# Optimization experiments

Hardware: AMD Instinct MI355X
Metric: run time of the kernel (lower is better)

## Reference

```python
import jax, jax.numpy as jnp
import numpy as np

B_SZ, SEQ = 16, 2048
VOCAB, EMBED = 50257, 128
DSTATE, HID, NCLS = 16, 256, 10
NEDGE = 8192  # edges per graph (avg degree 4)
LN_EPS = 1e-5


def setup_inputs() -> dict:
    key = jax.random.key(0)
    ks = jax.random.split(key, 12)
    tokens = jax.random.randint(ks[0], (B_SZ, SEQ), 0, VOCAB, dtype=jnp.int32)
    lengths = jnp.full((B_SZ,), SEQ, dtype=jnp.int32)  # full-length graphs
    edge_indices = jax.random.randint(ks[1], (B_SZ, 2, NEDGE), 0, SEQ, dtype=jnp.int32)
    emb = (jax.random.normal(ks[2], (VOCAB, EMBED)) * 0.02).at[0].set(0.0)  # padding_idx=0
    A_log = jax.random.normal(ks[3], (EMBED, DSTATE)) * 0.1
    B_w = jax.random.normal(ks[4], (DSTATE, EMBED)) * (1.0 / np.sqrt(EMBED))
    C_w = jax.random.normal(ks[5], (EMBED, DSTATE)) * (1.0 / np.sqrt(DSTATE))
    D_skip = jnp.ones((EMBED,))
    ln_g = jnp.ones((EMBED,))
    ln_b = jnp.zeros((EMBED,))
    Wmsg_w = jax.random.normal(ks[6], (HID, EMBED)) * (1.0 / np.sqrt(EMBED))
    Wupd_w = jax.random.normal(ks[7], (HID, EMBED + HID)) * (1.0 / np.sqrt(EMBED + HID))
    Wupd_b = jax.random.normal(ks[8], (HID,)) * 0.01
    cls_w = jax.random.normal(ks[9], (NCLS, HID)) * (1.0 / np.sqrt(HID))
    cls_b = jnp.zeros((NCLS,))
    return {"tokens": tokens, "lengths": lengths, "edge_indices": edge_indices,
            "emb": emb, "A_log": A_log, "B_w": B_w, "C_w": C_w, "D_skip": D_skip,
            "ln_g": ln_g, "ln_b": ln_b, "Wmsg_w": Wmsg_w, "Wupd_w": Wupd_w,
            "Wupd_b": Wupd_b, "cls_w": cls_w, "cls_b": cls_b}


def _ssm(x, A_log, B_w, C_w, D_skip, ln_g, ln_b):
    # x: (B, S, d_model). Diagonal SSM: h_t = h_{t-1}*exp(A) + B x_t (broadcast over d_model)
    Aexp = jnp.exp(-jnp.exp(A_log))  # (d_model, d_state)
    h0 = jnp.zeros((x.shape[0], EMBED, DSTATE), dtype=x.dtype)

    def step(h, x_t):  # x_t: (B, d_model)
        b_t = x_t @ B_w.T                            # (B, d_state)
        h = h * Aexp[None] + b_t[:, None, :]          # (B, d_model, d_state)
        y = h.mean(axis=1) @ C_w.T + D_skip * x_t     # (B, d_model)
        return h, y

    _, ys = jax.lax.scan(step, h0, jnp.swapaxes(x, 0, 1))
    out = jnp.swapaxes(ys, 0, 1)                      # (B, S, d_model)
    mu = out.mean(-1, keepdims=True)
    var = jnp.mean((out - mu) ** 2, axis=-1, keepdims=True)
    return ln_g * (out - mu) * jax.lax.rsqrt(var + LN_EPS) + ln_b


def reference(tokens, lengths, edge_indices, emb, A_log, B_w, C_w, D_skip,
              ln_g, ln_b, Wmsg_w, Wupd_w, Wupd_b, cls_w, cls_b):
    x = emb[tokens]                                   # (B, S, E)
    h = _ssm(x, A_log, B_w, C_w, D_skip, ln_g, ln_b)  # (B, S, E)
    src, dst = edge_indices[:, 0, :], edge_indices[:, 1, :]   # (B, Ne)
    h_src = jnp.take_along_axis(h, src[:, :, None], axis=1)   # (B, Ne, E)
    msgs = jnp.einsum('bed,hd->beh', h_src, Wmsg_w)            # (B, Ne, H)
    flat_dst = (jnp.arange(B_SZ, dtype=dst.dtype)[:, None] * SEQ + dst).reshape(-1)
    agg = jax.ops.segment_sum(msgs.reshape(-1, HID), flat_dst,
                              num_segments=B_SZ * SEQ).reshape(B_SZ, SEQ, HID)
    upd = jax.nn.relu(jnp.concatenate([h, agg], axis=-1) @ Wupd_w.T + Wupd_b)  # (B, S, H)
    pooled = upd.mean(axis=1)                          # (B, H)  (all lengths == SEQ)
    return pooled @ cls_w.T + cls_b                    # (B, NCLS)
```

## Files before the change

kernel.cpp:

```cpp
#include <hip/hip_runtime.h>

#define B_SZ   16
#define SEQ    2048
#define VOCAB  50257
#define EMBED  128
#define DSTATE 16
#define HID    256
#define NCLS   10
#define NEDGE  8192
#define KTR    64
#define LN_EPS 1e-5f
#define NROW   (B_SZ*SEQ)
#define BCAP   32
#define OVCAP  1024

#define PB_PRECM  128
#define PB_CTAB   (PB_PRECM + 16)
#define PB_TOTAL  (PB_CTAB + 1)

typedef float  f32x4 __attribute__((ext_vector_type(4)));
typedef short  s16x8 __attribute__((ext_vector_type(8)));

__device__ __forceinline__ float scrub(float x){
  return (x == x && fabsf(x) < 1e30f) ? x : 0.f;
}
__device__ __forceinline__ short f2b(float f){
  unsigned int u = __float_as_uint(f);
  unsigned int r = (u + 0x7fffu + ((u >> 16) & 1u)) >> 16;
  return (short)r;
}
__device__ __forceinline__ unsigned int pack2(float a, float b){
  return (unsigned int)(unsigned short)f2b(a)
       | ((unsigned int)(unsigned short)f2b(b) << 16);
}
__device__ __forceinline__ float lo2f(unsigned int v){ return __uint_as_float(v << 16); }
__device__ __forceinline__ float hi2f(unsigned int v){ return __uint_as_float(v & 0xffff0000u); }

__global__ __launch_bounds__(256) void k_prep(
    const float* __restrict__ A_log, const float* __restrict__ B_w,
    const float* __restrict__ Wmsg, const float* __restrict__ Wupd,
    float* __restrict__ c_tab, short* __restrict__ Bf, float* __restrict__ MT){
  int bid = blockIdx.x, tid = threadIdx.x;
  if (bid < PB_PRECM){
    int hp = bid*2 + (tid >> 7);
    int e  = tid & 127;
    const float* w2 = Wupd + (size_t)hp*384 + 128;
    float acc = 0.f;
    for (int h1 = 0; h1 < HID; ++h1)
      acc += Wmsg[h1*EMBED + e] * w2[h1];
    MT[(size_t)hp*EMBED + e] = scrub(acc);
  } else if (bid < PB_CTAB){
    if (tid < 64){
      int d = bid - PB_PRECM, lane = tid;
      float a0 = scrub(expf(-expf(A_log[(2*lane+0)*DSTATE + d])));
      float a1 = scrub(expf(-expf(A_log[(2*lane+1)*DSTATE + d])));
      float p0 = 1.f, p1 = 1.f;
      for (int k = 0; k < KTR; ++k){
        float s = p0 + p1;
        for (int off = 32; off; off >>= 1) s += __shfl_down(s, off);
        if (lane == 0) c_tab[k*DSTATE + d] = scrub(s * (1.0f/128.0f));
        p0 *= a0; p1 *= a1;
      }
    }
  } else {
    int idx = tid;
    int c = idx >> 6, lane = idx & 63;
    int n = lane & 15;
    int kb = c*32 + (lane >> 4)*8;
    short v[8];
    #pragma unroll
    for (int jj = 0; jj < 8; ++jj) v[jj] = f2b(B_w[(size_t)n*EMBED + kb + jj]);
    *(s16x8*)(Bf + (size_t)idx*8) = *(s16x8*)v;
  }
}

__global__ __launch_bounds__(256) void k_ssm_fused(
    const int* __restrict__ tokens, const float* __restrict__ emb,
    const float* __restrict__ c_tab,
    const float* __restrict__ C_w, const float* __restrict__ D_skip,
    const float* __restrict__ ln_g, const float* __restrict__ ln_b,
    const short* __restrict__ Bf, const float* __restrict__ Wupd,
    const float* __restrict__ MT, unsigned int* __restrict__ h_out,
    short* __restrict__ Wcs, const int* __restrict__ edges,
    int* __restrict__ cnt, unsigned short* __restrict__ bucket,
    int* __restrict__ ovf_cnt, int* __restrict__ ovf){
  __shared__ unsigned int xsh[128][68];
  __shared__ float bsh[128][18];
  __shared__ float msh[64][18];
  __shared__ float Ct[DSTATE][EMBED+2];
  __shared__ float csh[KTR][DSTATE];
  int bid = blockIdx.x, tid = threadIdx.x;

  if (bid >= 544){
    int eid = (bid-544)*256 + tid;
    int b2 = eid >> 13, i = eid & (NEDGE-1);
    const int* ei = edges + (size_t)b2*2*NEDGE;
    int s = ei[i]         & (SEQ-1);
    int d = ei[NEDGE + i] & (SEQ-1);
    int gdst = (b2 << 11) | d;
    int slot = atomicAdd(&cnt[gdst], 1);
    if (slot < BCAP) bucket[(size_t)gdst*BCAP + slot] = (unsigned short)s;
    else {
      int o = atomicAdd(ovf_cnt, 1);
      if (o < OVCAP) ovf[o] = ((b2 << 11) | s) | (gdst << 16);
    }
    return;
  }

  if (bid >= 512){
    int idx = (bid-512)*256 + tid;
    int c    = idx >> 10;
    int rem  = idx & 1023;
    int j    = rem >> 6;
    int lane = rem & 63;
    int n  = j*16 + (lane & 15);
    int kb = c*32 + (lane >> 4)*8;
    short v[8];
    #pragma unroll
    for (int jj = 0; jj < 8; ++jj){
      int k = kb + jj;
      float val = (k < 128) ? Wupd[(size_t)n*384 + k] : MT[(size_t)n*EMBED + (k-128)];
      v[jj] = f2b(val);
    }
    *(s16x8*)(Wcs + (size_t)idx*8) = *(s16x8*)v;
    return;
  }

  int b  = bid >> 5;
  int t0 = (bid & 31) * 64;

  {
    const int* tkb = tokens + b*SEQ;
    for (int i = 0; i < 16; ++i){
      int gid = i*256 + tid;
      int lr = gid >> 5, ch = gid & 31;
      int t = t0 - 64 + lr;
      uint2 o; o.x = 0u; o.y = 0u;
      if (t >= 0){
        int tok = tkb[t];
        tok = tok < 0 ? 0 : (tok >= VOCAB ? VOCAB-1 : tok);
        float4 v = *(const float4*)(emb + (size_t)tok*EMBED + ch*4);
        o.x = pack2(v.x, v.y); o.y = pack2(v.z, v.w);
      }
      *(uint2*)&xsh[lr][ch*2] = o;
    }
  }
  for (int i = tid; i < DSTATE*EMBED; i += 256){
    int e = i >> 4, d = i & 15;
    Ct[d][e] = C_w[i];
  }
  for (int i = tid; i < KTR*DSTATE; i += 256)
    csh[i >> 4][i & 15] = c_tab[i];
  __syncthreads();

  int wv = tid >> 6, lane = tid & 63;
  int m = lane & 15, lg = lane >> 4;

  const s16x8* Bp = (const s16x8*)Bf;
  #pragma unroll
  for (int tt = 0; tt < 2; ++tt){
    int tile = wv*2 + tt;
    int trow = t0 - 64 + tile*16;
    f32x4 acc = (f32x4){0.f,0.f,0.f,0.f};
    if (trow >= 0){
      const short* xrow = (const short*)&xsh[tile*16 + m][0] + lg*8;
      #pragma unroll
      for (int c = 0; c < 4; ++c){
        s16x8 a = *(const s16x8*)(xrow + c*32);
        acc = __builtin_amdgcn_mfma_f32_16x16x32_bf16(a, Bp[c*64 + lane], acc, 0, 0, 0);
      }
    }
    #pragma unroll
    for (int r = 0; r < 4; ++r)
      bsh[tile*16 + lg*4 + r][m] = scrub(acc[r]);
  }
  __syncthreads();

  {
    int d = tid & 15;
    #pragma unroll
    for (int it = 0; it < 4; ++it){
      int q = (tid + it*256) >> 4;
      int t = t0 + q;
      int base = 64 + q;
      int kmax = (t+1 < KTR) ? t+1 : KTR;
      float acc = 0.f;
      for (int k = 0; k < kmax; ++k) acc += csh[k][d] * bsh[base-k][d];
      msh[q][d] = scrub(acc);
    }
  }
  __syncthreads();

  int e0 = lane*2;
  float2 dsk = *(const float2*)&D_skip[e0];
  float2 lgv = *(const float2*)&ln_g[e0];
  float2 lbv = *(const float2*)&ln_b[e0];
  for (int q = wv*16; q < wv*16+16; ++q){
    int row = b*SEQ + t0 + q;
    unsigned int xp = xsh[64 + q][lane];
    float x0 = lo2f(xp), x1 = hi2f(xp);
    float y0 = dsk.x*x0, y1 = dsk.y*x1;
    #pragma unroll
    for (int d = 0; d < DSTATE; ++d){
      float md = msh[q][d];
      y0 += md * Ct[d][e0];
      y1 += md * Ct[d][e0+1];
    }
    y0 = scrub(y0); y1 = scrub(y1);
    float s = y0+y1, s2 = y0*y0 + y1*y1;
    for (int off = 32; off; off >>= 1){ s += __shfl_down(s,off); s2 += __shfl_down(s2,off); }
    s = __shfl(s, 0); s2 = __shfl(s2, 0);
    float mu  = s * (1.f/EMBED);
    float var = s2 * (1.f/EMBED) - mu*mu;
    float inv = rsqrtf(fmaxf(var, 0.f) + LN_EPS);
    float o0 = scrub(lgv.x*(y0-mu)*inv + lbv.x);
    float o1 = scrub(lgv.y*(y1-mu)*inv + lbv.y);
    h_out[(size_t)row*(EMBED/2) + lane] = pack2(o0, o1);
  }
}

__global__ __launch_bounds__(256) void k_gupd(
    const short* __restrict__ h, const int* __restrict__ cnt,
    const unsigned short* __restrict__ bucket,
    const int* __restrict__ ovf_cnt, const int* __restrict__ ovf,
    const short* __restrict__ Wcs, const float* __restrict__ Wupd_b,
    const float* __restrict__ cls_w, const float* __restrict__ cls_b,
    float* __restrict__ out){
  __shared__ unsigned int gsh[16][68];
  __shared__ float psum[HID];
  __shared__ float oacc[4][NCLS];
  int tid = threadIdx.x;
  int wv = tid >> 6, lane = tid & 63;
  int row0 = blockIdx.x * 16;
  int b = row0 >> 11;
  int m = lane & 15, lg = lane >> 4;

  const unsigned int* hb  = (const unsigned int*)h + (size_t)b*SEQ*(EMBED/2);
  const unsigned int* h32 = (const unsigned int*)h;
  int on = *ovf_cnt; on = on > OVCAP ? OVCAP : on;
  int hh = lane >> 5;
  int lw = lane & 31;
  for (int i = 0; i < 2; ++i){
    int rloc = wv*4 + i*2 + hh;
    int r = row0 + rloc;
    int n = cnt[r]; n = n > BCAP ? BCAP : n;
    const unsigned short* bk = bucket + (size_t)r*BCAP;
    float ax0=0.f, ay0=0.f, ax1=0.f, ay1=0.f;
    int t = 0;
    for (; t + 4 <= n; t += 4){
      ushort4 s4 = *(const ushort4*)(bk + t);
      uint2 v0 = *(const uint2*)&hb[(size_t)s4.x*(EMBED/2) + lw*2];
      uint2 v1 = *(const uint2*)&hb[(size_t)s4.y*(EMBED/2) + lw*2];
      uint2 v2 = *(const uint2*)&hb[(size_t)s4.z*(EMBED/2) + lw*2];
      uint2 v3 = *(const uint2*)&hb[(size_t)s4.w*(EMBED/2) + lw*2];
      ax0 += lo2f(v0.x); ay0 += hi2f(v0.x); ax1 += lo2f(v0.y); ay1 += hi2f(v0.y);
      ax0 += lo2f(v1.x); ay0 += hi2f(v1.x); ax1 += lo2f(v1.y); ay1 += hi2f(v1.y);
      ax0 += lo2f(v2.x); ay0 += hi2f(v2.x); ax1 += lo2f(v2.y); ay1 += hi2f(v2.y);
      ax0 += lo2f(v3.x); ay0 += hi2f(v3.x); ax1 += lo2f(v3.y); ay1 += hi2f(v3.y);
    }
    for (; t < n; ++t){
      uint2 v = *(const uint2*)&hb[(size_t)bk[t]*(EMBED/2) + lw*2];
      ax0 += lo2f(v.x); ay0 += hi2f(v.x); ax1 += lo2f(v.y); ay1 += hi2f(v.y);
    }
    for (int idx = 0; idx < on; ++idx){
      int pk = ovf[idx];
      if (((pk >> 16) & 0x7fff) == r){
        uint2 v = *(const uint2*)&h32[(size_t)(pk & 0xffff)*(EMBED/2) + lw*2];
        ax0 += lo2f(v.x); ay0 += hi2f(v.x); ax1 += lo2f(v.y); ay1 += hi2f(v.y);
      }
    }
    uint2 o; o.x = pack2(scrub(ax0), scrub(ay0));
    o.y = pack2(scrub(ax1), scrub(ay1));
    *(uint2*)&gsh[rloc][lw*2] = o;
  }
  __syncthreads();

  const short* hrow = h + (size_t)(row0+m)*EMBED + lg*8;
  s16x8 hfrag[4], gfrag[4];
  #pragma unroll
  for (int c = 0; c < 4; ++c){
    hfrag[c] = *(const s16x8*)(hrow + c*32);
    gfrag[c] = *(const s16x8*)&gsh[m][c*16 + lg*4];
  }

  int j0 = wv*4;
  f32x4 acc[4];
  #pragma unroll
  for (int jj = 0; jj < 4; ++jj) acc[jj] = (f32x4){0.f,0.f,0.f,0.f};
  const s16x8* Bp = (const s16x8*)Wcs;
  #pragma unroll
  for (int c = 0; c < 8; ++c){
    s16x8 a = (c < 4) ? hfrag[c] : gfrag[c-4];
    #pragma unroll
    for (int jj = 0; jj < 4; ++jj){
      s16x8 bfr = Bp[(c*16 + j0 + jj)*64 + lane];
      acc[jj] = __builtin_amdgcn_mfma_f32_16x16x32_bf16(a, bfr, acc[jj], 0, 0, 0);
    }
  }

  #pragma unroll
  for (int jj = 0; jj < 4; ++jj){
    int n = (j0 + jj)*16 + m;
    float bias = Wupd_b[n];
    float v = 0.f;
    #pragma unroll
    for (int r = 0; r < 4; ++r) v += fmaxf(acc[jj][r] + bias, 0.f);
    v += __shfl_down(v, 32);
    v += __shfl_down(v, 16);
    if (lane < 16) psum[n] = scrub(v);
  }
  __syncthreads();

  {
    float pn = psum[tid];
    #pragma unroll
    for (int c = 0; c < NCLS; ++c){
      float t = pn * cls_w[c*HID + tid];
      for (int off = 32; off; off >>= 1) t += __shfl_down(t, off);
      if (lane == 0) oacc[wv][c] = t;
    }
    __syncthreads();
    if (tid < NCLS){
      float s = oacc[0][tid] + oacc[1][tid] + oacc[2][tid] + oacc[3][tid];
      atomicAdd(&out[b*NCLS + tid], scrub(s * (1.0f/SEQ)));
    }
    if ((blockIdx.x & 127) == 0 && tid < NCLS)
      atomicAdd(&out[b*NCLS + tid], cls_b[tid]);
  }
}

extern "C" void kernel_launch(void* const* d_in, const int* in_sizes, int n_in,
                              void* d_out, int out_size, void* d_ws, size_t ws_size,
                              hipStream_t stream) {
  const int*   tokens = (const int*)d_in[0];
  const int*   edges  = (const int*)d_in[2];
  const float* emb    = (const float*)d_in[3];
  const float* A_log  = (const float*)d_in[4];
  const float* B_w    = (const float*)d_in[5];
  const float* C_w    = (const float*)d_in[6];
  const float* D_skip = (const float*)d_in[7];
  const float* ln_g   = (const float*)d_in[8];
  const float* ln_b   = (const float*)d_in[9];
  const float* Wmsg   = (const float*)d_in[10];
  const float* Wupd   = (const float*)d_in[11];
  const float* Wupd_b = (const float*)d_in[12];
  const float* cls_w  = (const float*)d_in[13];
  const float* cls_b  = (const float*)d_in[14];
  float* out = (float*)d_out;

  char* ws = (char*)d_ws;
  float* c_tab = (float*)ws;  ws += 16*1024;
  float* MT    = (float*)ws;  ws += (size_t)HID*EMBED*4;
  short* Wcs   = (short*)ws;  ws += (size_t)HID*HID*2;
  short* Bf    = (short*)ws;  ws += 16*1024;
  char*  zbase = ws;
  int*   cnt   = (int*)ws;    ws += (size_t)NROW*4;
  int*   ovf_cnt = (int*)ws;  ws += 64;
  int*   ovf   = (int*)ws;    ws += OVCAP*4;
  size_t zlen = (size_t)((char*)ws - zbase);
  unsigned short* bucket = (unsigned short*)ws; ws += (size_t)NROW*BCAP*2;
  short* h_bf  = (short*)ws;  ws += (size_t)NROW*EMBED*2;

  hipMemsetAsync(zbase, 0, zlen, stream);
  hipMemsetAsync(out, 0, (size_t)B_SZ*NCLS*4, stream);
  hipLaunchKernelGGL(k_prep, dim3(PB_TOTAL), dim3(256), 0, stream,
                     A_log, B_w, Wmsg, Wupd, c_tab, Bf, MT);
  hipLaunchKernelGGL(k_ssm_fused, dim3(1056), dim3(256), 0, stream,
                     tokens, emb, c_tab, C_w, D_skip, ln_g, ln_b, Bf, Wupd, MT,
                     (unsigned int*)h_bf, Wcs, edges, cnt, bucket, ovf_cnt, ovf);
  hipLaunchKernelGGL(k_gupd, dim3(NROW/16), dim3(256), 0, stream,
                     h_bf, cnt, bucket, ovf_cnt, ovf, Wcs, Wupd_b,
                     cls_w, cls_b, out);
}
```

Before: 179.9 us.

## Fold memsets into prep kernel, halve SSM tile size, keep C_w in registers

Replaces the two hipMemsetAsync calls with zeroing blocks inside the prep kernel, which removes two extra stream operations. The SSM main blocks now cover 32 timesteps instead of 64, doubling the block count to 1024 for better occupancy, at the cost of a proportionally larger 64-step halo reload per block. The C_w transpose in shared memory is replaced by per-thread register copies loaded straight from global memory. The zeroing covers cnt, ovf_cnt and ovf via a computed int count, so correctness depends on that size matching.

```diff
diff --git a/kernel.cpp b/kernel.cpp
--- a/kernel.cpp
+++ b/kernel.cpp
@@ -16,7 +16,15 @@
 
 #define PB_PRECM  128
 #define PB_CTAB   (PB_PRECM + 16)
-#define PB_TOTAL  (PB_CTAB + 1)
+#define PB_PRECB  (PB_CTAB + 1)
+#define PB_ZNINT  33808
+#define PB_ZBLK   34
+#define PB_ZOUT   (PB_PRECB + PB_ZBLK)
+#define PB_TOTAL  (PB_ZOUT + 1)
+
+#define SSM_MAIN  1024
+#define SSM_PRECW (SSM_MAIN + 32)
+#define SSM_TOTAL (SSM_PRECW + 512)
 
 typedef float  f32x4 __attribute__((ext_vector_type(4)));
 typedef short  s16x8 __attribute__((ext_vector_type(8)));
@@ -39,7 +47,8 @@
 __global__ __launch_bounds__(256) void k_prep(
     const float* __restrict__ A_log, const float* __restrict__ B_w,
     const float* __restrict__ Wmsg, const float* __restrict__ Wupd,
-    float* __restrict__ c_tab, short* __restrict__ Bf, float* __restrict__ MT){
+    float* __restrict__ c_tab, short* __restrict__ Bf, float* __restrict__ MT,
+    int* __restrict__ cnt, float* __restrict__ out){
   int bid = blockIdx.x, tid = threadIdx.x;
   if (bid < PB_PRECM){
     int hp = bid*2 + (tid >> 7);
@@ -62,7 +71,7 @@
         p0 *= a0; p1 *= a1;
       }
     }
-  } else {
+  } else if (bid < PB_PRECB){
     int idx = tid;
     int c = idx >> 6, lane = idx & 63;
     int n = lane & 15;
@@ -71,6 +80,14 @@
     #pragma unroll
     for (int jj = 0; jj < 8; ++jj) v[jj] = f2b(B_w[(size_t)n*EMBED + kb + jj]);
     *(s16x8*)(Bf + (size_t)idx*8) = *(s16x8*)v;
+  } else if (bid < PB_ZOUT){
+    int idx4 = (bid-PB_PRECB)*1024 + tid*4;
+    if (idx4 < PB_ZNINT){
+      uint4 z; z.x = z.y = z.z = z.w = 0u;
+      *(uint4*)&cnt[idx4] = z;
+    }
+  } else {
+    if (tid < B_SZ*NCLS) out[tid] = 0.f;
   }
 }
 
@@ -84,15 +101,14 @@
     short* __restrict__ Wcs, const int* __restrict__ edges,
     int* __restrict__ cnt, unsigned short* __restrict__ bucket,
     int* __restrict__ ovf_cnt, int* __restrict__ ovf){
-  __shared__ unsigned int xsh[128][68];
-  __shared__ float bsh[128][18];
-  __shared__ float msh[64][18];
-  __shared__ float Ct[DSTATE][EMBED+2];
+  __shared__ unsigned int xsh[96][68];
+  __shared__ float bsh[96][18];
+  __shared__ float msh[32][18];
   __shared__ float csh[KTR][DSTATE];
   int bid = blockIdx.x, tid = threadIdx.x;
 
-  if (bid >= 544){
-    int eid = (bid-544)*256 + tid;
+  if (bid >= SSM_PRECW){
+    int eid = (bid-SSM_PRECW)*256 + tid;
     int b2 = eid >> 13, i = eid & (NEDGE-1);
     const int* ei = edges + (size_t)b2*2*NEDGE;
     int s = ei[i]         & (SEQ-1);
@@ -107,8 +123,8 @@
     return;
   }
 
-  if (bid >= 512){
-    int idx = (bid-512)*256 + tid;
+  if (bid >= SSM_MAIN){
+    int idx = (bid-SSM_MAIN)*256 + tid;
     int c    = idx >> 10;
     int rem  = idx & 1023;
     int j    = rem >> 6;
@@ -126,12 +142,15 @@
     return;
   }
 
-  int b  = bid >> 5;
-  int t0 = (bid & 31) * 64;
+  int b  = bid >> 6;
+  int t0 = (bid & 63) * 32;
+  int wv = tid >> 6, lane = tid & 63;
+  int m = lane & 15, lg = lane >> 4;
 
   {
     const int* tkb = tokens + b*SEQ;
-    for (int i = 0; i < 16; ++i){
+    #pragma unroll
+    for (int i = 0; i < 12; ++i){
       int gid = i*256 + tid;
       int lr = gid >> 5, ch = gid & 31;
       int t = t0 - 64 + lr;
@@ -145,41 +164,49 @@
       *(uint2*)&xsh[lr][ch*2] = o;
     }
   }
-  for (int i = tid; i < DSTATE*EMBED; i += 256){
-    int e = i >> 4, d = i & 15;
-    Ct[d][e] = C_w[i];
-  }
   for (int i = tid; i < KTR*DSTATE; i += 256)
     csh[i >> 4][i & 15] = c_tab[i];
-  __syncthreads();
-
-  int wv = tid >> 6, lane = tid & 63;
-  int m = lane & 15, lg = lane >> 4;
+
+  int e0 = lane*2;
+  float ct0[DSTATE], ct1[DSTATE];
+  {
+    const float4* c0 = (const float4*)(C_w + (size_t)e0*DSTATE);
+    const float4* c1 = (const float4*)(C_w + (size_t)(e0+1)*DSTATE);
+    #pragma unroll
+    for (int i = 0; i < 4; ++i){
+      float4 v0 = c0[i], v1 = c1[i];
+      ct0[i*4+0]=v0.x; ct0[i*4+1]=v0.y; ct0[i*4+2]=v0.z; ct0[i*4+3]=v0.w;
+      ct1[i*4+0]=v1.x; ct1[i*4+1]=v1.y; ct1[i*4+2]=v1.z; ct1[i*4+3]=v1.w;
+    }
+  }
+  __syncthreads();
 
   const s16x8* Bp = (const s16x8*)Bf;
   #pragma unroll
   for (int tt = 0; tt < 2; ++tt){
     int tile = wv*2 + tt;
-    int trow = t0 - 64 + tile*16;
-    f32x4 acc = (f32x4){0.f,0.f,0.f,0.f};
-    if (trow >= 0){
-      const short* xrow = (const short*)&xsh[tile*16 + m][0] + lg*8;
+    if (tile < 6){
+      int trow = t0 - 64 + tile*16;
+      f32x4 acc = (f32x4){0.f,0.f,0.f,0.f};
+      if (trow >= 0){
+        const short* xrow = (const short*)&xsh[tile*16 + m][0] + lg*8;
+        #pragma unroll
+        for (int c = 0; c < 4; ++c){
+          s16x8 a = *(const s16x8*)(xrow + c*32);
+          acc = __builtin_amdgcn_mfma_f32_16x16x32_bf16(a, Bp[c*64 + lane], acc, 0, 0, 0);
+        }
+      }
       #pragma unroll
-      for (int c = 0; c < 4; ++c){
-        s16x8 a = *(const s16x8*)(xrow + c*32);
-        acc = __builtin_amdgcn_mfma_f32_16x16x32_bf16(a, Bp[c*64 + lane], acc, 0, 0, 0);
-      }
-    }
-    #pragma unroll
-    for (int r = 0; r < 4; ++r)
-      bsh[tile*16 + lg*4 + r][m] = scrub(acc[r]);
+      for (int r = 0; r < 4; ++r)
+        bsh[tile*16 + lg*4 + r][m] = scrub(acc[r]);
+    }
   }
   __syncthreads();
 
   {
     int d = tid & 15;
     #pragma unroll
-    for (int it = 0; it < 4; ++it){
+    for (int it = 0; it < 2; ++it){
       int q = (tid + it*256) >> 4;
       int t = t0 + q;
       int base = 64 + q;
@@ -191,11 +218,10 @@
   }
   __syncthreads();
 
-  int e0 = lane*2;
   float2 dsk = *(const float2*)&D_skip[e0];
   float2 lgv = *(const float2*)&ln_g[e0];
   float2 lbv = *(const float2*)&ln_b[e0];
-  for (int q = wv*16; q < wv*16+16; ++q){
+  for (int q = wv*8; q < wv*8+8; ++q){
     int row = b*SEQ + t0 + q;
     unsigned int xp = xsh[64 + q][lane];
     float x0 = lo2f(xp), x1 = hi2f(xp);
@@ -203,8 +229,8 @@
     #pragma unroll
     for (int d = 0; d < DSTATE; ++d){
       float md = msh[q][d];
-      y0 += md * Ct[d][e0];
-      y1 += md * Ct[d][e0+1];
+      y0 += md * ct0[d];
+      y1 += md * ct1[d];
     }
     y0 = scrub(y0); y1 = scrub(y1);
     float s = y0+y1, s2 = y0*y0 + y1*y1;
@@ -353,19 +379,15 @@
   float* MT    = (float*)ws;  ws += (size_t)HID*EMBED*4;
   short* Wcs   = (short*)ws;  ws += (size_t)HID*HID*2;
   short* Bf    = (short*)ws;  ws += 16*1024;
-  char*  zbase = ws;
   int*   cnt   = (int*)ws;    ws += (size_t)NROW*4;
   int*   ovf_cnt = (int*)ws;  ws += 64;
   int*   ovf   = (int*)ws;    ws += OVCAP*4;
-  size_t zlen = (size_t)((char*)ws - zbase);
   unsigned short* bucket = (unsigned short*)ws; ws += (size_t)NROW*BCAP*2;
   short* h_bf  = (short*)ws;  ws += (size_t)NROW*EMBED*2;
 
-  hipMemsetAsync(zbase, 0, zlen, stream);
-  hipMemsetAsync(out, 0, (size_t)B_SZ*NCLS*4, stream);
   hipLaunchKernelGGL(k_prep, dim3(PB_TOTAL), dim3(256), 0, stream,
-                     A_log, B_w, Wmsg, Wupd, c_tab, Bf, MT);
-  hipLaunchKernelGGL(k_ssm_fused, dim3(1056), dim3(256), 0, stream,
+                     A_log, B_w, Wmsg, Wupd, c_tab, Bf, MT, cnt, out);
+  hipLaunchKernelGGL(k_ssm_fused, dim3(SSM_TOTAL), dim3(256), 0, stream,
                      tokens, emb, c_tab, C_w, D_skip, ln_g, ln_b, Bf, Wupd, MT,
                      (unsigned int*)h_bf, Wcs, edges, cnt, bucket, ovf_cnt, ovf);
   hipLaunchKernelGGL(k_gupd, dim3(NROW/16), dim3(256), 0, stream,
```

New measurement: 175.7 us. 1.02x faster.
